# Optimization experiments

Measured on AMD Instinct MI355X. Metric: run time of the kernel, lower is better.

## Reference

```python
import jax, jax.numpy as jnp
import numpy as np

TAU0 = 0.5  # Concrete temperature (init kwarg tau0)
EPS = float(np.finfo(np.float32).eps)  # torch.finfo(float32).eps clamp


def _linear_params(key, fan_in, fan_out):
    # matches torch nn.Linear default init: U(-1/sqrt(fan_in), 1/sqrt(fan_in))
    bound = 1.0 / np.sqrt(fan_in)
    kw, kb = jax.random.split(key)
    W = jax.random.uniform(kw, (fan_in, fan_out), minval=-bound, maxval=bound, dtype=jnp.float32)
    b = jax.random.uniform(kb, (fan_out,), minval=-bound, maxval=bound, dtype=jnp.float32)
    return W, b


def setup_inputs() -> dict:
    key = jax.random.key(0)
    ks = jax.random.split(key, 6)
    B, D, K = 32768, 200, 10
    w1, b1 = _linear_params(ks[0], D, 100)    # dense1
    w2, b2 = _linear_params(ks[1], 100, 100)  # dense2
    wl, bl = _linear_params(ks[2], 100, D)    # logits
    wo, bo = _linear_params(ks[3], D, 2)      # output (requires D == 200)
    x = jax.random.normal(ks[4], (B, D), dtype=jnp.float32)
    uniform = jax.random.uniform(ks[5], (B, K, D), dtype=jnp.float32)
    return {"x": x, "uniform": uniform,
            "w1": w1, "b1": b1, "w2": w2, "b2": b2,
            "wl": wl, "bl": bl, "wo": wo, "bo": bo}


def reference(x, uniform, w1, b1, w2, b2, wl, bl, wo, bo):
    # selector MLP
    h = jax.nn.relu(x @ w1 + b1)            # (B, 100)
    h = jax.nn.relu(h @ w2 + b2)            # (B, 100)
    logits = h @ wl + bl                    # (B, D)
    # SampleConcrete (training path): gumbel-softmax over features, max over k samples
    u = jnp.clip(uniform, EPS, 1.0)         # (B, K, D)
    gumbel = -jnp.log(-jnp.log(u))
    noisy = (gumbel + logits[:, None, :]) / TAU0
    samples = jax.nn.softmax(noisy, axis=-1).max(axis=1)  # (B, D); repeat_count == 1
    xs = x * samples
    preds = jax.nn.softmax(xs @ wo + bo, axis=-1)          # (B, 2)
    # hsic(xs, preds) in the original is computed but discarded -> omitted
    return preds, samples
```

## Files before the change

kernel.cpp:

```cpp
#include <hip/hip_runtime.h>
#include <hip/hip_bf16.h>

__launch_bounds__(256)
__global__ void fused_mlp12(const float* __restrict__ x,
                            const float* __restrict__ w1, const float* __restrict__ b1,
                            const float* __restrict__ w2, const float* __restrict__ b2,
                            float* __restrict__ h2out) {
  constexpr int BM = 64, KC = 20, BMP = 68;
  __shared__ float At[KC * BMP];
  __shared__ float Ws[KC * 128];
  __shared__ float h1T[100 * BMP];

  const int t = threadIdx.x;
  const int tx = t & 31;
  const int ty = t >> 5;
  const int rowBase = blockIdx.x * BM;

  float acc[8][4];
#pragma unroll
  for (int i = 0; i < 8; i++)
#pragma unroll
    for (int j = 0; j < 4; j++) acc[i][j] = 0.0f;

  for (int kc = 0; kc < 200; kc += KC) {
#pragma unroll
    for (int i = t; i < BM * KC; i += 256) {
      int r = i / KC, k = i - r * KC;
      At[k * BMP + r] = x[(rowBase + r) * 200 + kc + k];
    }
#pragma unroll
    for (int i = t; i < KC * 128; i += 256) {
      int k = i >> 7, c = i & 127;
      Ws[i] = (c < 100) ? w1[(kc + k) * 100 + c] : 0.0f;
    }
    __syncthreads();
#pragma unroll
    for (int k = 0; k < KC; k++) {
      float a[8], b[4];
      *(float4*)&a[0] = *(const float4*)&At[k * BMP + ty * 8];
      *(float4*)&a[4] = *(const float4*)&At[k * BMP + ty * 8 + 4];
      *(float4*)&b[0] = *(const float4*)&Ws[k * 128 + tx * 4];
#pragma unroll
      for (int i = 0; i < 8; i++)
#pragma unroll
        for (int j = 0; j < 4; j++) acc[i][j] += a[i] * b[j];
    }
    __syncthreads();
  }

  if (tx < 25) {
#pragma unroll
    for (int i = 0; i < 8; i++) {
      const int r = ty * 8 + i;
#pragma unroll
      for (int j = 0; j < 4; j++) {
        const int c = tx * 4 + j;
        h1T[c * BMP + r] = fmaxf(acc[i][j] + b1[c], 0.0f);
      }
    }
  }
  __syncthreads();

#pragma unroll
  for (int i = 0; i < 8; i++)
#pragma unroll
    for (int j = 0; j < 4; j++) acc[i][j] = 0.0f;

  for (int kc = 0; kc < 100; kc += KC) {
#pragma unroll
    for (int i = t; i < KC * 128; i += 256) {
      int k = i >> 7, c = i & 127;
      Ws[i] = (c < 100) ? w2[(kc + k) * 100 + c] : 0.0f;
    }
    __syncthreads();
#pragma unroll
    for (int k = 0; k < KC; k++) {
      float a[8], b[4];
      *(float4*)&a[0] = *(const float4*)&h1T[(kc + k) * BMP + ty * 8];
      *(float4*)&a[4] = *(const float4*)&h1T[(kc + k) * BMP + ty * 8 + 4];
      *(float4*)&b[0] = *(const float4*)&Ws[k * 128 + tx * 4];
#pragma unroll
      for (int i = 0; i < 8; i++)
#pragma unroll
        for (int j = 0; j < 4; j++) acc[i][j] += a[i] * b[j];
    }
    __syncthreads();
  }

  if (tx < 25) {
#pragma unroll
    for (int i = 0; i < 8; i++) {
      const int r = rowBase + ty * 8 + i;
      float4 v;
      v.x = fmaxf(acc[i][0] + b2[tx * 4 + 0], 0.0f);
      v.y = fmaxf(acc[i][1] + b2[tx * 4 + 1], 0.0f);
      v.z = fmaxf(acc[i][2] + b2[tx * 4 + 2], 0.0f);
      v.w = fmaxf(acc[i][3] + b2[tx * 4 + 3], 0.0f);
      *(float4*)&h2out[r * 100 + tx * 4] = v;
    }
  }
}

__launch_bounds__(512, 4)
__global__ void fused_logits_concrete(const float* __restrict__ x,
                                      const float* __restrict__ uniform,
                                      const float* __restrict__ h2,
                                      const float* __restrict__ wl, const float* __restrict__ bl,
                                      const float* __restrict__ wo, const float* __restrict__ bo,
                                      float* __restrict__ out, int B) {
  constexpr int BM = 64, KC = 20, BMP = 68;
  constexpr float EPS = 1.1920929e-07f;
  __shared__ float At[KC * BMP];
  __shared__ float Ws[KC * 256];
  __shared__ float lg[BM * 200];

  const int t = threadIdx.x;
  const int rowBase = blockIdx.x * BM;

  {
    const int tx = t & 31;
    const int ty = t >> 5;
    float acc[4][8];
#pragma unroll
    for (int i = 0; i < 4; i++)
#pragma unroll
      for (int j = 0; j < 8; j++) acc[i][j] = 0.0f;

    for (int kc = 0; kc < 100; kc += KC) {
      for (int i = t; i < BM * KC; i += 512) {
        int r = i / KC, k = i - r * KC;
        At[k * BMP + r] = h2[(rowBase + r) * 100 + kc + k];
      }
#pragma unroll
      for (int i = t; i < KC * 256; i += 512) {
        int k = i >> 8, c = i & 255;
        Ws[i] = (c < 200) ? wl[(kc + k) * 200 + c] : 0.0f;
      }
      __syncthreads();
#pragma unroll
      for (int k = 0; k < KC; k++) {
        float a[4], b[8];
        *(float4*)&a[0] = *(const float4*)&At[k * BMP + ty * 4];
        *(float4*)&b[0] = *(const float4*)&Ws[k * 256 + tx * 8];
        *(float4*)&b[4] = *(const float4*)&Ws[k * 256 + tx * 8 + 4];
#pragma unroll
        for (int i = 0; i < 4; i++)
#pragma unroll
          for (int j = 0; j < 8; j++) acc[i][j] += a[i] * b[j];
      }
      __syncthreads();
    }

    if (tx < 25) {
#pragma unroll
      for (int i = 0; i < 4; i++) {
        const int r = ty * 4 + i;
        float4 v0, v1;
        v0.x = acc[i][0] + bl[tx * 8 + 0];
        v0.y = acc[i][1] + bl[tx * 8 + 1];
        v0.z = acc[i][2] + bl[tx * 8 + 2];
        v0.w = acc[i][3] + bl[tx * 8 + 3];
        v1.x = acc[i][4] + bl[tx * 8 + 4];
        v1.y = acc[i][5] + bl[tx * 8 + 5];
        v1.z = acc[i][6] + bl[tx * 8 + 6];
        v1.w = acc[i][7] + bl[tx * 8 + 7];
        *(float4*)&lg[r * 200 + tx * 8] = v0;
        *(float4*)&lg[r * 200 + tx * 8 + 4] = v1;
      }
    }
    __syncthreads();
  }

  const int lane = t & 63;
  const int wave = t >> 6;
  const int samplesBase = B * 2;

#pragma unroll 1
  for (int rr = 0; rr < 8; rr++) {
    const int r = wave * 8 + rr;
    const int b = rowBase + r;

    float lgv[4], xv[4], smax[4];
#pragma unroll
    for (int i = 0; i < 4; i++) {
      const int d = lane + 64 * i;
      const bool v = (d < 200);
      lgv[i] = v ? lg[r * 200 + d] : 0.0f;
      xv[i] = v ? x[(size_t)b * 200 + d] : 0.0f;
      smax[i] = 0.0f;
    }

    const float* __restrict__ u = uniform + (size_t)b * 2000;
    float uu[10][4];
#pragma unroll
    for (int k = 0; k < 10; k++)
#pragma unroll
      for (int i = 0; i < 4; i++) {
        const int d = lane + 64 * i;
        uu[k][i] = (d < 200) ? u[k * 200 + d] : 0.5f;
      }

#pragma unroll
    for (int k = 0; k < 10; k++) {
      float noisy[4];
      float mloc = -1e30f;
#pragma unroll
      for (int i = 0; i < 4; i++) {
        if (lane + 64 * i < 200) {
          float uc = fminf(fmaxf(uu[k][i], EPS), 1.0f);
          const float g = -__logf(-__logf(uc));
          noisy[i] = (g + lgv[i]) * 2.0f;
          mloc = fmaxf(mloc, noisy[i]);
        } else {
          noisy[i] = -1e30f;
        }
      }
#pragma unroll
      for (int off = 32; off > 0; off >>= 1)
        mloc = fmaxf(mloc, __shfl_xor(mloc, off, 64));

      float e[4], ssum = 0.0f;
#pragma unroll
      for (int i = 0; i < 4; i++) {
        e[i] = (lane + 64 * i < 200) ? __expf(noisy[i] - mloc) : 0.0f;
        ssum += e[i];
      }
#pragma unroll
      for (int off = 32; off > 0; off >>= 1)
        ssum += __shfl_xor(ssum, off, 64);

      const float inv = 1.0f / ssum;
#pragma unroll
      for (int i = 0; i < 4; i++) smax[i] = fmaxf(smax[i], e[i] * inv);
    }

    float p0 = 0.0f, p1 = 0.0f;
#pragma unroll
    for (int i = 0; i < 4; i++) {
      const int d = lane + 64 * i;
      if (d < 200) {
        const float s = smax[i];
        out[samplesBase + (size_t)b * 200 + d] = s;
        const float xs = xv[i] * s;
        p0 += xs * wo[d * 2 + 0];
        p1 += xs * wo[d * 2 + 1];
      }
    }
#pragma unroll
    for (int off = 32; off > 0; off >>= 1) {
      p0 += __shfl_xor(p0, off, 64);
      p1 += __shfl_xor(p1, off, 64);
    }
    if (lane == 0) {
      const float z0 = p0 + bo[0];
      const float z1 = p1 + bo[1];
      const float m = fmaxf(z0, z1);
      const float e0 = __expf(z0 - m);
      const float e1 = __expf(z1 - m);
      out[b * 2 + 0] = e0 / (e0 + e1);
      out[b * 2 + 1] = e1 / (e0 + e1);
    }
  }
}

extern "C" void kernel_launch(void* const* d_in, const int* in_sizes, int n_in,
                              void* d_out, int out_size, void* d_ws, size_t ws_size,
                              hipStream_t stream) {
  const float* x  = (const float*)d_in[0];
  const float* un = (const float*)d_in[1];
  const float* w1 = (const float*)d_in[2];
  const float* b1 = (const float*)d_in[3];
  const float* w2 = (const float*)d_in[4];
  const float* b2 = (const float*)d_in[5];
  const float* wl = (const float*)d_in[6];
  const float* bl = (const float*)d_in[7];
  const float* wo = (const float*)d_in[8];
  const float* bo = (const float*)d_in[9];
  float* out = (float*)d_out;

  const int B = in_sizes[0] / 200;
  float* h2 = (float*)d_ws;

  fused_mlp12<<<B / 64, 256, 0, stream>>>(x, w1, b1, w2, b2, h2);
  fused_logits_concrete<<<B / 64, 512, 0, stream>>>(x, un, h2, wl, bl, wo, bo, out, B);
}
```

Before: 566.2 us.

## Fuse all MLP layers and concrete sampling into one kernel with 8-lane row groups

Merges the two kernels into one, so h1 and h2 stay in shared memory instead of making a round trip through a global workspace, and one launch is removed. The concrete sampling stage is reorganised so each row is handled by an 8-lane group using float4 loads. This replaces the old scheme of one wave per row looping over 8 rows with full 64-lane shuffles. Output weights are staged in shared memory. Shared memory use grows to about 120KB per block, which limits occupancy, and each thread now keeps many more values live in registers.

```diff
diff --git a/kernel.cpp b/kernel.cpp
--- a/kernel.cpp
+++ b/kernel.cpp
@@ -1,265 +1,229 @@
 #include <hip/hip_runtime.h>
-#include <hip/hip_bf16.h>
-
-__launch_bounds__(256)
-__global__ void fused_mlp12(const float* __restrict__ x,
-                            const float* __restrict__ w1, const float* __restrict__ b1,
-                            const float* __restrict__ w2, const float* __restrict__ b2,
-                            float* __restrict__ h2out) {
-  constexpr int BM = 64, KC = 20, BMP = 68;
-  __shared__ float At[KC * BMP];
-  __shared__ float Ws[KC * 128];
-  __shared__ float h1T[100 * BMP];
-
-  const int t = threadIdx.x;
-  const int tx = t & 31;
-  const int ty = t >> 5;
-  const int rowBase = blockIdx.x * BM;
-
-  float acc[8][4];
-#pragma unroll
-  for (int i = 0; i < 8; i++)
-#pragma unroll
-    for (int j = 0; j < 4; j++) acc[i][j] = 0.0f;
-
-  for (int kc = 0; kc < 200; kc += KC) {
-#pragma unroll
-    for (int i = t; i < BM * KC; i += 256) {
-      int r = i / KC, k = i - r * KC;
-      At[k * BMP + r] = x[(rowBase + r) * 200 + kc + k];
-    }
-#pragma unroll
-    for (int i = t; i < KC * 128; i += 256) {
-      int k = i >> 7, c = i & 127;
-      Ws[i] = (c < 100) ? w1[(kc + k) * 100 + c] : 0.0f;
-    }
-    __syncthreads();
-#pragma unroll
-    for (int k = 0; k < KC; k++) {
-      float a[8], b[4];
-      *(float4*)&a[0] = *(const float4*)&At[k * BMP + ty * 8];
-      *(float4*)&a[4] = *(const float4*)&At[k * BMP + ty * 8 + 4];
-      *(float4*)&b[0] = *(const float4*)&Ws[k * 128 + tx * 4];
-#pragma unroll
-      for (int i = 0; i < 8; i++)
-#pragma unroll
-        for (int j = 0; j < 4; j++) acc[i][j] += a[i] * b[j];
-    }
-    __syncthreads();
-  }
-
-  if (tx < 25) {
-#pragma unroll
-    for (int i = 0; i < 8; i++) {
-      const int r = ty * 8 + i;
-#pragma unroll
-      for (int j = 0; j < 4; j++) {
-        const int c = tx * 4 + j;
-        h1T[c * BMP + r] = fmaxf(acc[i][j] + b1[c], 0.0f);
-      }
-    }
-  }
-  __syncthreads();
-
-#pragma unroll
-  for (int i = 0; i < 8; i++)
-#pragma unroll
-    for (int j = 0; j < 4; j++) acc[i][j] = 0.0f;
-
-  for (int kc = 0; kc < 100; kc += KC) {
-#pragma unroll
-    for (int i = t; i < KC * 128; i += 256) {
-      int k = i >> 7, c = i & 127;
-      Ws[i] = (c < 100) ? w2[(kc + k) * 100 + c] : 0.0f;
-    }
-    __syncthreads();
-#pragma unroll
-    for (int k = 0; k < KC; k++) {
-      float a[8], b[4];
-      *(float4*)&a[0] = *(const float4*)&h1T[(kc + k) * BMP + ty * 8];
-      *(float4*)&a[4] = *(const float4*)&h1T[(kc + k) * BMP + ty * 8 + 4];
-      *(float4*)&b[0] = *(const float4*)&Ws[k * 128 + tx * 4];
-#pragma unroll
-      for (int i = 0; i < 8; i++)
-#pragma unroll
-        for (int j = 0; j < 4; j++) acc[i][j] += a[i] * b[j];
-    }
-    __syncthreads();
-  }
-
-  if (tx < 25) {
-#pragma unroll
-    for (int i = 0; i < 8; i++) {
-      const int r = rowBase + ty * 8 + i;
-      float4 v;
-      v.x = fmaxf(acc[i][0] + b2[tx * 4 + 0], 0.0f);
-      v.y = fmaxf(acc[i][1] + b2[tx * 4 + 1], 0.0f);
-      v.z = fmaxf(acc[i][2] + b2[tx * 4 + 2], 0.0f);
-      v.w = fmaxf(acc[i][3] + b2[tx * 4 + 3], 0.0f);
-      *(float4*)&h2out[r * 100 + tx * 4] = v;
-    }
-  }
-}
-
-__launch_bounds__(512, 4)
-__global__ void fused_logits_concrete(const float* __restrict__ x,
-                                      const float* __restrict__ uniform,
-                                      const float* __restrict__ h2,
-                                      const float* __restrict__ wl, const float* __restrict__ bl,
-                                      const float* __restrict__ wo, const float* __restrict__ bo,
-                                      float* __restrict__ out, int B) {
-  constexpr int BM = 64, KC = 20, BMP = 68;
+
+#define FI4(p) (*(const float4*)(p))
+
+__launch_bounds__(512, 2)
+__global__ void l2x_fused(const float* __restrict__ x,
+                          const float* __restrict__ uniform,
+                          const float* __restrict__ w1, const float* __restrict__ b1,
+                          const float* __restrict__ w2, const float* __restrict__ b2,
+                          const float* __restrict__ wl, const float* __restrict__ bl,
+                          const float* __restrict__ wo, const float* __restrict__ bo,
+                          float* __restrict__ out, int B) {
+  constexpr int BMP = 68;
+  constexpr int KC = 20;
+  constexpr int LGS = 204;
   constexpr float EPS = 1.1920929e-07f;
+
   __shared__ float At[KC * BMP];
   __shared__ float Ws[KC * 256];
-  __shared__ float lg[BM * 200];
+  __shared__ float h1T[100 * BMP];
+  __shared__ float h2T[100 * BMP];
+  __shared__ float lg[64 * LGS];
+  __shared__ float woS[400];
+  __shared__ float boS[2];
 
   const int t = threadIdx.x;
-  const int rowBase = blockIdx.x * BM;
+  const int tx = t & 31, ty = t >> 5;
+  const int rowBase = blockIdx.x * 64;
+
+  if (t < 400) woS[t] = wo[t];
+  if (t < 2) boS[t] = bo[t];
 
   {
-    const int tx = t & 31;
-    const int ty = t >> 5;
-    float acc[4][8];
-#pragma unroll
-    for (int i = 0; i < 4; i++)
-#pragma unroll
-      for (int j = 0; j < 8; j++) acc[i][j] = 0.0f;
-
+    float acc[4][4] = {};
+    for (int kc = 0; kc < 200; kc += KC) {
+      for (int i = t; i < 64 * KC; i += 512) {
+        int r = i / KC, k = i - r * KC;
+        At[k * BMP + r] = x[(size_t)(rowBase + r) * 200 + kc + k];
+      }
+      for (int i = t; i < KC * 128; i += 512) {
+        int k = i >> 7, c = i & 127;
+        Ws[k * 128 + c] = (c < 100) ? w1[(kc + k) * 100 + c] : 0.0f;
+      }
+      __syncthreads();
+#pragma unroll
+      for (int k = 0; k < KC; k++) {
+        float a[4], bq[4];
+        *(float4*)a = FI4(&At[k * BMP + ty * 4]);
+        *(float4*)bq = FI4(&Ws[k * 128 + tx * 4]);
+#pragma unroll
+        for (int i = 0; i < 4; i++)
+#pragma unroll
+          for (int j = 0; j < 4; j++) acc[i][j] = fmaf(a[i], bq[j], acc[i][j]);
+      }
+      __syncthreads();
+    }
+    if (tx < 25) {
+      float bv[4];
+#pragma unroll
+      for (int j = 0; j < 4; j++) bv[j] = b1[tx * 4 + j];
+#pragma unroll
+      for (int i = 0; i < 4; i++) {
+        int r = ty * 4 + i;
+#pragma unroll
+        for (int j = 0; j < 4; j++)
+          h1T[(tx * 4 + j) * BMP + r] = fmaxf(acc[i][j] + bv[j], 0.0f);
+      }
+    }
+  }
+
+  {
+    float acc[4][4] = {};
     for (int kc = 0; kc < 100; kc += KC) {
-      for (int i = t; i < BM * KC; i += 512) {
-        int r = i / KC, k = i - r * KC;
-        At[k * BMP + r] = h2[(rowBase + r) * 100 + kc + k];
-      }
-#pragma unroll
+      for (int i = t; i < KC * 128; i += 512) {
+        int k = i >> 7, c = i & 127;
+        Ws[k * 128 + c] = (c < 100) ? w2[(kc + k) * 100 + c] : 0.0f;
+      }
+      __syncthreads();
+#pragma unroll
+      for (int k = 0; k < KC; k++) {
+        float a[4], bq[4];
+        *(float4*)a = FI4(&h1T[(kc + k) * BMP + ty * 4]);
+        *(float4*)bq = FI4(&Ws[k * 128 + tx * 4]);
+#pragma unroll
+        for (int i = 0; i < 4; i++)
+#pragma unroll
+          for (int j = 0; j < 4; j++) acc[i][j] = fmaf(a[i], bq[j], acc[i][j]);
+      }
+      __syncthreads();
+    }
+    if (tx < 25) {
+      float bv[4];
+#pragma unroll
+      for (int j = 0; j < 4; j++) bv[j] = b2[tx * 4 + j];
+#pragma unroll
+      for (int i = 0; i < 4; i++) {
+        int r = ty * 4 + i;
+#pragma unroll
+        for (int j = 0; j < 4; j++)
+          h2T[(tx * 4 + j) * BMP + r] = fmaxf(acc[i][j] + bv[j], 0.0f);
+      }
+    }
+  }
+
+  {
+    float acc[4][8] = {};
+    for (int kc = 0; kc < 100; kc += KC) {
       for (int i = t; i < KC * 256; i += 512) {
         int k = i >> 8, c = i & 255;
-        Ws[i] = (c < 200) ? wl[(kc + k) * 200 + c] : 0.0f;
+        Ws[k * 256 + c] = (c < 200) ? wl[(kc + k) * 200 + c] : 0.0f;
       }
       __syncthreads();
 #pragma unroll
       for (int k = 0; k < KC; k++) {
-        float a[4], b[8];
-        *(float4*)&a[0] = *(const float4*)&At[k * BMP + ty * 4];
-        *(float4*)&b[0] = *(const float4*)&Ws[k * 256 + tx * 8];
-        *(float4*)&b[4] = *(const float4*)&Ws[k * 256 + tx * 8 + 4];
+        float a[4], bq[8];
+        *(float4*)a = FI4(&h2T[(kc + k) * BMP + ty * 4]);
+        *(float4*)&bq[0] = FI4(&Ws[k * 256 + tx * 8]);
+        *(float4*)&bq[4] = FI4(&Ws[k * 256 + tx * 8 + 4]);
 #pragma unroll
         for (int i = 0; i < 4; i++)
 #pragma unroll
-          for (int j = 0; j < 8; j++) acc[i][j] += a[i] * b[j];
-      }
-      __syncthreads();
-    }
-
+          for (int j = 0; j < 8; j++) acc[i][j] = fmaf(a[i], bq[j], acc[i][j]);
+      }
+      __syncthreads();
+    }
     if (tx < 25) {
+      float bv[8];
+#pragma unroll
+      for (int j = 0; j < 8; j++) bv[j] = bl[tx * 8 + j];
 #pragma unroll
       for (int i = 0; i < 4; i++) {
-        const int r = ty * 4 + i;
+        int r = ty * 4 + i;
         float4 v0, v1;
-        v0.x = acc[i][0] + bl[tx * 8 + 0];
-        v0.y = acc[i][1] + bl[tx * 8 + 1];
-        v0.z = acc[i][2] + bl[tx * 8 + 2];
-        v0.w = acc[i][3] + bl[tx * 8 + 3];
-        v1.x = acc[i][4] + bl[tx * 8 + 4];
-        v1.y = acc[i][5] + bl[tx * 8 + 5];
-        v1.z = acc[i][6] + bl[tx * 8 + 6];
-        v1.w = acc[i][7] + bl[tx * 8 + 7];
-        *(float4*)&lg[r * 200 + tx * 8] = v0;
-        *(float4*)&lg[r * 200 + tx * 8 + 4] = v1;
-      }
-    }
-    __syncthreads();
-  }
+        v0.x = acc[i][0] + bv[0]; v0.y = acc[i][1] + bv[1];
+        v0.z = acc[i][2] + bv[2]; v0.w = acc[i][3] + bv[3];
+        v1.x = acc[i][4] + bv[4]; v1.y = acc[i][5] + bv[5];
+        v1.z = acc[i][6] + bv[6]; v1.w = acc[i][7] + bv[7];
+        *(float4*)&lg[r * LGS + tx * 8] = v0;
+        *(float4*)&lg[r * LGS + tx * 8 + 4] = v1;
+      }
+    }
+  }
+  __syncthreads();
 
   const int lane = t & 63;
-  const int wave = t >> 6;
-  const int samplesBase = B * 2;
-
-#pragma unroll 1
-  for (int rr = 0; rr < 8; rr++) {
-    const int r = wave * 8 + rr;
-    const int b = rowBase + r;
-
-    float lgv[4], xv[4], smax[4];
-#pragma unroll
-    for (int i = 0; i < 4; i++) {
-      const int d = lane + 64 * i;
-      const bool v = (d < 200);
-      lgv[i] = v ? lg[r * 200 + d] : 0.0f;
-      xv[i] = v ? x[(size_t)b * 200 + d] : 0.0f;
-      smax[i] = 0.0f;
-    }
-
-    const float* __restrict__ u = uniform + (size_t)b * 2000;
-    float uu[10][4];
-#pragma unroll
-    for (int k = 0; k < 10; k++)
-#pragma unroll
-      for (int i = 0; i < 4; i++) {
-        const int d = lane + 64 * i;
-        uu[k][i] = (d < 200) ? u[k * 200 + d] : 0.5f;
-      }
-
-#pragma unroll
-    for (int k = 0; k < 10; k++) {
-      float noisy[4];
-      float mloc = -1e30f;
-#pragma unroll
-      for (int i = 0; i < 4; i++) {
-        if (lane + 64 * i < 200) {
-          float uc = fminf(fmaxf(uu[k][i], EPS), 1.0f);
-          const float g = -__logf(-__logf(uc));
-          noisy[i] = (g + lgv[i]) * 2.0f;
-          mloc = fmaxf(mloc, noisy[i]);
-        } else {
-          noisy[i] = -1e30f;
-        }
-      }
-#pragma unroll
-      for (int off = 32; off > 0; off >>= 1)
-        mloc = fmaxf(mloc, __shfl_xor(mloc, off, 64));
-
-      float e[4], ssum = 0.0f;
-#pragma unroll
-      for (int i = 0; i < 4; i++) {
-        e[i] = (lane + 64 * i < 200) ? __expf(noisy[i] - mloc) : 0.0f;
-        ssum += e[i];
-      }
-#pragma unroll
-      for (int off = 32; off > 0; off >>= 1)
-        ssum += __shfl_xor(ssum, off, 64);
-
-      const float inv = 1.0f / ssum;
-#pragma unroll
-      for (int i = 0; i < 4; i++) smax[i] = fmaxf(smax[i], e[i] * inv);
-    }
-
-    float p0 = 0.0f, p1 = 0.0f;
-#pragma unroll
-    for (int i = 0; i < 4; i++) {
-      const int d = lane + 64 * i;
-      if (d < 200) {
-        const float s = smax[i];
-        out[samplesBase + (size_t)b * 200 + d] = s;
-        const float xs = xv[i] * s;
-        p0 += xs * wo[d * 2 + 0];
-        p1 += xs * wo[d * 2 + 1];
-      }
-    }
-#pragma unroll
-    for (int off = 32; off > 0; off >>= 1) {
-      p0 += __shfl_xor(p0, off, 64);
-      p1 += __shfl_xor(p1, off, 64);
-    }
-    if (lane == 0) {
-      const float z0 = p0 + bo[0];
-      const float z1 = p1 + bo[1];
-      const float m = fmaxf(z0, z1);
-      const float e0 = __expf(z0 - m);
-      const float e1 = __expf(z1 - m);
-      out[b * 2 + 0] = e0 / (e0 + e1);
-      out[b * 2 + 1] = e1 / (e0 + e1);
-    }
+  const int wv = t >> 6;
+  const int g = lane >> 3, sub = lane & 7;
+  const int r = wv * 8 + g;
+  const int b = rowBase + r;
+  const bool full = (sub < 2);
+
+  float4 lgv[7], smax[7];
+#pragma unroll
+  for (int jj = 0; jj < 6; jj++) {
+    lgv[jj] = FI4(&lg[r * LGS + jj * 32 + sub * 4]);
+    smax[jj] = make_float4(0.f, 0.f, 0.f, 0.f);
+  }
+  lgv[6] = full ? FI4(&lg[r * LGS + 192 + sub * 4]) : make_float4(0.f, 0.f, 0.f, 0.f);
+  smax[6] = make_float4(0.f, 0.f, 0.f, 0.f);
+
+  const float* __restrict__ ub = uniform + (size_t)b * 2000;
+  float* smf = (float*)smax;
+  const float* lgf = (const float*)lgv;
+
+#pragma unroll
+  for (int k = 0; k < 10; k++) {
+    float4 u[7];
+#pragma unroll
+    for (int jj = 0; jj < 6; jj++) u[jj] = FI4(ub + k * 200 + jj * 32 + sub * 4);
+    u[6] = full ? FI4(ub + k * 200 + 192 + sub * 4) : make_float4(0.5f, 0.5f, 0.5f, 0.5f);
+
+    float* uf = (float*)u;
+    float mloc = -1e30f;
+#pragma unroll
+    for (int e = 0; e < 28; e++) {
+      float uc = fminf(fmaxf(uf[e], EPS), 1.0f);
+      float nz = (-__logf(-__logf(uc)) + lgf[e]) * 2.0f;
+      if (e >= 24) nz = full ? nz : -1e30f;
+      uf[e] = nz;
+      mloc = fmaxf(mloc, nz);
+    }
+    mloc = fmaxf(mloc, __shfl_xor(mloc, 1));
+    mloc = fmaxf(mloc, __shfl_xor(mloc, 2));
+    mloc = fmaxf(mloc, __shfl_xor(mloc, 4));
+
+    float ss = 0.0f;
+#pragma unroll
+    for (int e = 0; e < 28; e++) {
+      float ev = __expf(uf[e] - mloc);
+      uf[e] = ev;
+      ss += ev;
+    }
+    ss += __shfl_xor(ss, 1);
+    ss += __shfl_xor(ss, 2);
+    ss += __shfl_xor(ss, 4);
+
+    const float inv = 1.0f / ss;
+#pragma unroll
+    for (int e = 0; e < 28; e++) smf[e] = fmaxf(smf[e], uf[e] * inv);
+  }
+
+  float p0 = 0.0f, p1 = 0.0f;
+#pragma unroll
+  for (int jj = 0; jj < 7; jj++) {
+    if (jj < 6 || full) {
+      const int d0 = jj * 32 + sub * 4;
+      *(float4*)(out + (size_t)2 * B + (size_t)b * 200 + d0) = smax[jj];
+      float4 xv = FI4(x + (size_t)b * 200 + d0);
+      float4 wa = FI4(&woS[2 * d0]);
+      float4 wb = FI4(&woS[2 * d0 + 4]);
+      const float xs0 = xv.x * smax[jj].x, xs1 = xv.y * smax[jj].y;
+      const float xs2 = xv.z * smax[jj].z, xs3 = xv.w * smax[jj].w;
+      p0 += xs0 * wa.x + xs1 * wa.z + xs2 * wb.x + xs3 * wb.z;
+      p1 += xs0 * wa.y + xs1 * wa.w + xs2 * wb.y + xs3 * wb.w;
+    }
+  }
+  p0 += __shfl_xor(p0, 1); p0 += __shfl_xor(p0, 2); p0 += __shfl_xor(p0, 4);
+  p1 += __shfl_xor(p1, 1); p1 += __shfl_xor(p1, 2); p1 += __shfl_xor(p1, 4);
+  if (sub == 0) {
+    const float z0 = p0 + boS[0];
+    const float z1 = p1 + boS[1];
+    const float m = fmaxf(z0, z1);
+    const float e0 = __expf(z0 - m);
+    const float e1 = __expf(z1 - m);
+    const float s = e0 + e1;
+    *(float2*)(out + (size_t)b * 2) = make_float2(e0 / s, e1 / s);
   }
 }
 
@@ -279,8 +243,6 @@
   float* out = (float*)d_out;
 
   const int B = in_sizes[0] / 200;
-  float* h2 = (float*)d_ws;
-
-  fused_mlp12<<<B / 64, 256, 0, stream>>>(x, w1, b1, w2, b2, h2);
-  fused_logits_concrete<<<B / 64, 512, 0, stream>>>(x, un, h2, wl, bl, wo, bo, out, B);
+
+  l2x_fused<<<B / 64, 512, 0, stream>>>(x, un, w1, b1, w2, b2, wl, bl, wo, bo, out, B);
 }
```

After: 612.7 us. +8.2%, slower.
